# Kernel tuning notes

Measured on AMD Instinct MI355X. Metric: run time of the kernel, lower is better.

The kernel has to match this reference:

```python
import jax
import jax.numpy as jnp
from jax import lax
import numpy as np

EMBED_DIM = 768
NUM_HEADS = 12
BATCH = 8
SEQ = 1024
EPS = 1e-07
QK_QBIT = 8
QK_KBIT = 8
AV_ABIT = 8
AV_VBIT = 8
PROJ_WBIT = 8
PROJ_XBIT = 8
SCALE = EMBED_DIM ** (-0.5)  # module uses embed_dim, not head_dim


def _ste(hard, soft):
    # straight-through estimator: forward = hard, backward grad = d(soft)
    return soft + lax.stop_gradient(hard - soft)


def fake_quant_signed(x, bit):
    # _quantize_signed_matrix_train: sign/abs, global-max scaling, STE clamp + round
    sign = lax.stop_gradient(jnp.sign(x))
    a = jnp.abs(x)
    scaling = lax.stop_gradient(jnp.max(a)) + EPS
    y = a / scaling
    y = _ste(jnp.clip(y, 0.0, 1.0), y)          # Clamp.apply (STE)
    levels = 2.0 ** (bit - 1.0) - 1.0
    y = _ste(jnp.round(y * levels) / levels, y)  # Round.apply (STE)
    return y * scaling * sign


def fake_quant_unsigned(x, bit):
    # _quantize_unsigned_matrix_train
    scaling = lax.stop_gradient(jnp.max(x)) + EPS
    y = x / scaling
    y = _ste(jnp.clip(y, 0.0, 1.0), y)
    levels = 2.0 ** bit - 1.0
    y = _ste(jnp.round(y * levels) / levels, y)
    return y * scaling


def asim_linear(x, w, b, wbit, xbit):
    # ASiMLinear in 'Train' mode with signed_act=True: fake-quantize activation
    # and weight, dense matmul, trim_noise=0 -> no perturbation.
    xq = fake_quant_signed(x, xbit)
    wq = fake_quant_signed(w, wbit)
    return jnp.einsum('bnc,oc->bno', xq, wq) + b


def setup_inputs() -> dict:
    key = jax.random.key(0)
    k_x, k_qw, k_qb, k_pw, k_pb = jax.random.split(key, 5)
    x = jax.random.normal(k_x, (BATCH, SEQ, EMBED_DIM), dtype=jnp.float32)
    s = 1.0 / np.sqrt(EMBED_DIM)
    qkv_w = jax.random.normal(k_qw, (3 * EMBED_DIM, EMBED_DIM), dtype=jnp.float32) * s
    qkv_b = jax.random.normal(k_qb, (3 * EMBED_DIM,), dtype=jnp.float32) * 0.01
    proj_w = jax.random.normal(k_pw, (EMBED_DIM, EMBED_DIM), dtype=jnp.float32) * s
    proj_b = jax.random.normal(k_pb, (EMBED_DIM,), dtype=jnp.float32) * 0.01
    return {'x': x, 'qkv_w': qkv_w, 'qkv_b': qkv_b, 'proj_w': proj_w, 'proj_b': proj_b}


def reference(x, qkv_w, qkv_b, proj_w, proj_b):
    B, N, C = x.shape
    H = NUM_HEADS
    D = C // H
    # qkv projection (ASiMLinear, Train mode)
    qkv = asim_linear(x, qkv_w, qkv_b, PROJ_WBIT, PROJ_XBIT)      # [B, N, 3C]
    qkv = qkv.reshape(B, N, 3, H, D).transpose(2, 0, 3, 1, 4)      # [3, B, H, N, D]
    q, k, v = qkv[0], qkv[1], qkv[2]
    # _qk_train: fake-quantize q and k^T, matmul (trim_noise=0 -> no perturb)
    qq = fake_quant_signed(q, QK_QBIT)
    kq = fake_quant_signed(jnp.swapaxes(k, -2, -1), QK_KBIT)
    attn = jnp.einsum('bhnd,bhdm->bhnm', qq, kq) * SCALE           # [B, H, N, N]
    attn = jax.nn.softmax(attn, axis=-1)
    # dropout ratio 0.0 -> identity
    # _av_train: unsigned fake-quant of attention, signed fake-quant of v
    aq = fake_quant_unsigned(attn, AV_ABIT)
    vq = fake_quant_signed(v, AV_VBIT)
    out = jnp.einsum('bhnm,bhmd->bhnd', aq, vq)                    # [B, H, N, D]
    out = out.transpose(0, 2, 1, 3).reshape(B, N, C)
    # output projection (ASiMLinear, Train mode)
    out = asim_linear(out, proj_w, proj_b, PROJ_WBIT, PROJ_XBIT)
    return out
```

## Files before the change

kernel.cpp:

```cpp
#include <hip/hip_runtime.h>
#include <hip/hip_bf16.h>
#include <cstdint>
#include <cstddef>

#define B_    8
#define SEQ_  1024
#define C_    768
#define H_    12
#define D_    64
#define TC_   2304
#define M_    8192
#define EPS_  1e-7f
#define SCALE_ 0.036084391824351615f

typedef __attribute__((ext_vector_type(8))) short bf16x8;
typedef __attribute__((ext_vector_type(4))) float f32x4;
typedef __attribute__((ext_vector_type(4))) int   i32x4;

__device__ __forceinline__ bf16x8 expand8(int2 raw) {
  union { int2 v; signed char c[8]; } u; u.v = raw;
  bf16x8 r;
  #pragma unroll
  for (int j = 0; j < 8; ++j) {
    float f = (float)(int)u.c[j];
    r[j] = (short)(__float_as_uint(f) >> 16);
  }
  return r;
}
__device__ __forceinline__ void expand16(int4 raw, int4& lo, int4& hi) {
  union { int4 v; signed char c[16]; } u; u.v = raw;
  unsigned short s[16];
  #pragma unroll
  for (int j = 0; j < 16; ++j) {
    float f = (float)(int)u.c[j];
    s[j] = (unsigned short)(__float_as_uint(f) >> 16);
  }
  lo = *(const int4*)&s[0]; hi = *(const int4*)&s[8];
}

__device__ __forceinline__ int8_t quant1(float v, float s) {
  float y = fminf(fabsf(v) / s, 1.0f);
  int q = (int)rintf(y * 127.0f);
  return (int8_t)(v < 0.f ? -q : q);
}

__global__ void k_init(float* g) {
  if (threadIdx.x == 0) {
    g[0]=0.f; g[1]=0.f; g[2]=0.f; g[3]=0.f; g[4]=0.f; g[5]=0.f;
    g[6]=3.402823466e+38f;
    g[7]=0.f;
  }
}

__global__ __launch_bounds__(256) void k_absmax_fused(const float4* __restrict__ x,
                                                      const float4* __restrict__ w1,
                                                      const float4* __restrict__ w2,
                                                      float* g) {
  __shared__ float red[4];
  const int blk = blockIdx.x;
  const float4* p; unsigned n4; float* gout; int b0, nb;
  if (blk < 384)      { p = x;  n4 = 1572864u; gout = &g[0]; b0 = 0;   nb = 384; }
  else if (blk < 480) { p = w1; n4 = 442368u;  gout = &g[1]; b0 = 384; nb = 96;  }
  else                { p = w2; n4 = 147456u;  gout = &g[2]; b0 = 480; nb = 48;  }
  float m = 0.f;
  for (unsigned i = (unsigned)(blk - b0) * 256u + threadIdx.x; i < n4; i += (unsigned)nb * 256u) {
    float4 v = p[i];
    m = fmaxf(m, fmaxf(fmaxf(fabsf(v.x), fabsf(v.y)), fmaxf(fabsf(v.z), fabsf(v.w))));
  }
  #pragma unroll
  for (int off = 32; off; off >>= 1) m = fmaxf(m, __shfl_xor(m, off));
  if ((threadIdx.x & 63) == 0) red[threadIdx.x >> 6] = m;
  __syncthreads();
  if (threadIdx.x == 0) {
    m = fmaxf(fmaxf(red[0], red[1]), fmaxf(red[2], red[3]));
    atomicMax((unsigned int*)gout, __float_as_uint(m));
  }
}

__device__ __forceinline__ void quant_seg8(const float* __restrict__ in, unsigned n, float s,
                                           int8_t* __restrict__ out, unsigned i0, unsigned stride) {
  for (unsigned i = i0; i < n; i += stride)
    out[i] = quant1(in[i], s);
}
__global__ __launch_bounds__(256) void k_quant_fused(const float* __restrict__ x,
                                                     const float* __restrict__ w1,
                                                     const float* __restrict__ w2,
                                                     const float* __restrict__ g,
                                                     int8_t* __restrict__ xq,
                                                     int8_t* __restrict__ wq,
                                                     int8_t* __restrict__ pw) {
  const int blk = blockIdx.x;
  if (blk < 1536)      quant_seg8(x,  6291456u, g[0] + EPS_, xq, (unsigned)blk * 256u + threadIdx.x, 1536u * 256u);
  else if (blk < 1968) quant_seg8(w1, 1769472u, g[1] + EPS_, wq, (unsigned)(blk - 1536) * 256u + threadIdx.x, 432u * 256u);
  else                 quant_seg8(w2,  589824u, g[2] + EPS_, pw, (unsigned)(blk - 1968) * 256u + threadIdx.x, 144u * 256u);
}

__global__ __launch_bounds__(256) void k_quant_i8(const float* __restrict__ in, unsigned n,
                                                  const float* __restrict__ gmax,
                                                  int8_t* __restrict__ out) {
  const float s = *gmax + EPS_;
  quant_seg8(in, n, s, out, blockIdx.x * blockDim.x + threadIdx.x, gridDim.x * blockDim.x);
}

__global__ __launch_bounds__(256) void k_gemm8i(const int8_t* __restrict__ A,
                                                const int8_t* __restrict__ Bt,
                                                const float* __restrict__ bias,
                                                float* __restrict__ C,
                                                int Mn, int Nn, int Kn,
                                                const float* __restrict__ sA, const float* __restrict__ sB,
                                                float* pmax, int partDiv) {
  __shared__ int8_t As[4][128][16];
  __shared__ int8_t Bs[4][128][16];
  const int tid = threadIdx.x;
  int flat = blockIdx.y * gridDim.x + blockIdx.x;
  int chunk = (gridDim.x * gridDim.y) >> 3;
  int nf = (flat & 7) * chunk + (flat >> 3);
  const int n0 = (nf % gridDim.x) * 128, m0 = (nf / gridDim.x) * 128;
  const int wid = tid >> 6, lane = tid & 63;
  const int wr = wid >> 1, wc = wid & 1;
  const int lrow = lane & 15;
  const int lslot = lane >> 4;
  i32x4 acc[4][4] = {};
  const int srow = tid & 127;
  const int slot0 = tid >> 7;
  const int8_t* ga = A  + (size_t)(m0 + srow) * Kn + slot0 * 16;
  const int8_t* gb = Bt + (size_t)(n0 + srow) * Kn + slot0 * 16;
  const int nt = Kn >> 6;
  int4 ra0 = *(const int4*)(ga);
  int4 ra1 = *(const int4*)(ga + 32);
  int4 rb0 = *(const int4*)(gb);
  int4 rb1 = *(const int4*)(gb + 32);
  for (int t = 0; t < nt; ++t) {
    if (t) __syncthreads();
    *(int4*)&As[slot0][srow][0]     = ra0;
    *(int4*)&As[slot0 + 2][srow][0] = ra1;
    *(int4*)&Bs[slot0][srow][0]     = rb0;
    *(int4*)&Bs[slot0 + 2][srow][0] = rb1;
    if (t + 1 < nt) {
      const int ko = (t + 1) * 64;
      ra0 = *(const int4*)(ga + ko);
      ra1 = *(const int4*)(ga + ko + 32);
      rb0 = *(const int4*)(gb + ko);
      rb1 = *(const int4*)(gb + ko + 32);
    }
    __syncthreads();
    i32x4 af[4], bfr[4];
    #pragma unroll
    for (int i = 0; i < 4; ++i) af[i]  = *(const i32x4*)&As[lslot][wr * 64 + i * 16 + lrow][0];
    #pragma unroll
    for (int j = 0; j < 4; ++j) bfr[j] = *(const i32x4*)&Bs[lslot][wc * 64 + j * 16 + lrow][0];
    #pragma unroll
    for (int i = 0; i < 4; ++i)
      #pragma unroll
      for (int j = 0; j < 4; ++j)
        acc[i][j] = __builtin_amdgcn_mfma_i32_16x16x64_i8(af[i], bfr[j], acc[i][j], 0, 0, 0);
  }
  const float alpha = (sA[0] + EPS_) * (sB[0] + EPS_) * (1.0f / 16129.0f);
  const int orow = (lane >> 4) << 2;
  float amax = 0.f;
  #pragma unroll
  for (int i = 0; i < 4; ++i) {
    #pragma unroll
    for (int j = 0; j < 4; ++j) {
      int col = n0 + wc * 64 + j * 16 + lrow;
      float bc = bias[col];
      #pragma unroll
      for (int rr = 0; rr < 4; ++rr) {
        int row = m0 + wr * 64 + i * 16 + orow + rr;
        float val = (float)acc[i][j][rr] * alpha + bc;
        C[(size_t)row * Nn + col] = val;
        amax = fmaxf(amax, fabsf(val));
      }
    }
  }
  if (pmax) {
    #pragma unroll
    for (int off = 32; off; off >>= 1) amax = fmaxf(amax, __shfl_xor(amax, off));
    if (lane == 0) atomicMax((unsigned int*)&pmax[n0 / partDiv], __float_as_uint(amax));
  }
}

__global__ __launch_bounds__(256) void k_quant_heads(const float* __restrict__ qkvf, const float* __restrict__ g,
                                                     int8_t* __restrict__ qo, int8_t* __restrict__ ko,
                                                     int8_t* __restrict__ vT) {
  __shared__ float vt[64][65];
  const int bh = blockIdx.x >> 4, nt = blockIdx.x & 15;
  const int b = bh / 12, h = bh % 12;
  const int n0 = nt * 64;
  const int tid = threadIdx.x;
  const float s0 = g[3] + EPS_, s1 = g[4] + EPS_, s2 = g[5] + EPS_;
  const int r = tid >> 2, dc = tid & 3;
  const size_t mrow = (size_t)(b * 1024 + n0 + r) * 2304;
  union { int4 v; int8_t c[16]; } pk;
  {
    const float* src = qkvf + mrow + h * 64 + dc * 16;
    #pragma unroll
    for (int e = 0; e < 16; ++e) pk.c[e] = quant1(src[e], s0);
    *(int4*)&qo[((size_t)bh * 1024 + n0 + r) * 64 + dc * 16] = pk.v;
  }
  {
    const float* src = qkvf + mrow + 768 + h * 64 + dc * 16;
    #pragma unroll
    for (int e = 0; e < 16; ++e) pk.c[e] = quant1(src[e], s1);
    *(int4*)&ko[((size_t)bh * 1024 + n0 + r) * 64 + dc * 16] = pk.v;
  }
  {
    const float* src = qkvf + mrow + 1536 + h * 64 + dc * 16;
    #pragma unroll
    for (int e = 0; e < 16; ++e) vt[dc * 16 + e][r] = src[e];
  }
  __syncthreads();
  {
    const int d = tid >> 2, nc = tid & 3;
    #pragma unroll
    for (int e = 0; e < 16; ++e) pk.c[e] = quant1(vt[d][nc * 16 + e], s2);
    *(int4*)&vT[((size_t)bh * 64 + d) * 1024 + n0 + nc * 16] = pk.v;
  }
}

__global__ __launch_bounds__(256) void k_attn_stats_mfma(
    const int8_t* __restrict__ qi8, const int8_t* __restrict__ ki8,
    const float* __restrict__ g, float* __restrict__ rowmax, float* __restrict__ denomv,
    unsigned int* __restrict__ gminden) {
  __shared__ unsigned short Ks[64 * 64];
  __shared__ float red[4];
  const int bh = blockIdx.x >> 4, rt = blockIdx.x & 15;
  const int tid = threadIdx.x, w = tid >> 6, lane = tid & 63;
  const int lrow = lane & 15, lko = (lane >> 4) << 3;
  const int8_t* qbase = qi8 + (size_t)bh * 65536;
  const int8_t* kbase = ki8 + (size_t)bh * 65536;
  bf16x8 qf[2];
  #pragma unroll
  for (int ks = 0; ks < 2; ++ks)
    qf[ks] = expand8(*(const int2*)(qbase + (size_t)(rt*64 + w*16 + lrow) * 64 + ks*32 + lko));
  const float qkScale = (g[3] + EPS_) * (g[4] + EPS_) * (1.0f / 16129.0f) * SCALE_;
  float m = -3.0e38f, den = 0.f;
  const int srow = tid >> 2, sc = tid & 3;
  const int sx = (srow & 7) << 4;
  int4 kraw = *(const int4*)(kbase + (size_t)srow * 64 + sc * 16);
  for (int t = 0; t < 16; ++t) {
    __syncthreads();
    {
      int4 lo, hi; expand16(kraw, lo, hi);
      int bb = srow * 128 + sc * 32;
      *(int4*)((char*)Ks + ( bb       ^ sx)) = lo;
      *(int4*)((char*)Ks + ((bb + 16) ^ sx)) = hi;
    }
    if (t < 15)
      kraw = *(const int4*)(kbase + (size_t)(t + 1) * 4096 + (size_t)srow * 64 + sc * 16);
    __syncthreads();
    f32x4 acc[4] = {};
    #pragma unroll
    for (int ks = 0; ks < 2; ++ks)
      #pragma unroll
      for (int j = 0; j < 4; ++j) {
        int row = j * 16 + lrow;
        bf16x8 kf = *(const bf16x8*)((const char*)Ks + ((row * 128 + (ks*32 + lko) * 2) ^ ((row & 7) << 4)));
        acc[j] = __builtin_amdgcn_mfma_f32_16x16x32_bf16(kf, qf[ks], acc[j], 0, 0, 0);
      }
    float mnew = m;
    #pragma unroll
    for (int j = 0; j < 4; ++j)
      #pragma unroll
      for (int rr = 0; rr < 4; ++rr)
        mnew = fmaxf(mnew, acc[j][rr] * qkScale);
    float d = den * __expf(m - mnew);
    #pragma unroll
    for (int j = 0; j < 4; ++j)
      #pragma unroll
      for (int rr = 0; rr < 4; ++rr)
        d += __expf(acc[j][rr] * qkScale - mnew);
    den = d; m = mnew;
  }
  #pragma unroll
  for (int off = 16; off <= 32; off <<= 1) {
    float mo = __shfl_xor(m, off);
    float doo = __shfl_xor(den, off);
    float mg = fmaxf(m, mo);
    den = den * __expf(m - mg) + doo * __expf(mo - mg);
    m = mg;
  }
  if (lane < 16) {
    size_t rg = (size_t)bh * 1024 + rt * 64 + w * 16 + lane;
    rowmax[rg] = m;
    denomv[rg] = den;
  }
  float bm = den;
  #pragma unroll
  for (int off = 1; off < 16; off <<= 1) bm = fminf(bm, __shfl_xor(bm, off));
  if (lane == 0) red[w] = bm;
  __syncthreads();
  if (tid == 0)
    atomicMin(gminden, __float_as_uint(fminf(fminf(red[0], red[1]), fminf(red[2], red[3]))));
}

__global__ __launch_bounds__(256) void k_attn_pv_mfma(
    const int8_t* __restrict__ qi8, const int8_t* __restrict__ ki8, const int8_t* __restrict__ vti8,
    const float* __restrict__ g, const unsigned int* __restrict__ gminden,
    const float* __restrict__ rowmax, const float* __restrict__ denomv,
    float* __restrict__ aof, float* __restrict__ gamax) {
  __shared__ unsigned short Ks[64 * 64];
  __shared__ unsigned short Vs[64 * 64];
  __shared__ unsigned short Ps[64 * 64];
  __shared__ float red[4];
  const int bh = blockIdx.x >> 4, rt = blockIdx.x & 15;
  const int b = bh / 12, h = bh % 12;
  const int tid = threadIdx.x, w = tid >> 6, lane = tid & 63;
  const int lrow = lane & 15, lko = (lane >> 4) << 3;
  const int8_t* qbase = qi8 + (size_t)bh * 65536;
  const int8_t* kbase = ki8 + (size_t)bh * 65536;
  const int8_t* vbase = vti8 + (size_t)bh * 65536;
  bf16x8 qf[2];
  #pragma unroll
  for (int ks = 0; ks < 2; ++ks)
    qf[ks] = expand8(*(const int2*)(qbase + (size_t)(rt*64 + w*16 + lrow) * 64 + ks*32 + lko));
  const float qkScale = (g[3] + EPS_) * (g[4] + EPS_) * (1.0f / 16129.0f) * SCALE_;
  const float minden = __uint_as_float(*gminden);
  const float sa = 1.0f / minden + EPS_;
  const float invSa = 1.0f / sa;
  const float sv = g[5] + EPS_;
  const float pvScale = sa * sv * (1.0f / 32385.0f);
  const float rm  = rowmax[(size_t)bh * 1024 + rt * 64 + w * 16 + lrow];
  const float ivd = 1.0f / denomv[(size_t)bh * 1024 + rt * 64 + w * 16 + lrow];
  f32x4 accO[4] = {};
  const int srow = tid >> 2, sc = tid & 3;
  const int sx = (srow & 7) << 4;
  int4 kraw = *(const int4*)(kbase + (size_t)srow * 64 + sc * 16);
  int4 vraw = *(const int4*)(vbase + (size_t)srow * 1024 + sc * 16);
  for (int t = 0; t < 16; ++t) {
    __syncthreads();
    {
      int4 lo, hi;
      int bb = srow * 128 + sc * 32;
      expand16(kraw, lo, hi);
      *(int4*)((char*)Ks + ( bb       ^ sx)) = lo;
      *(int4*)((char*)Ks + ((bb + 16) ^ sx)) = hi;
      expand16(vraw, lo, hi);
      *(int4*)((char*)Vs + ( bb       ^ sx)) = lo;
      *(int4*)((char*)Vs + ((bb + 16) ^ sx)) = hi;
    }
    if (t < 15) {
      kraw = *(const int4*)(kbase + (size_t)(t + 1) * 4096 + (size_t)srow * 64 + sc * 16);
      vraw = *(const int4*)(vbase + (size_t)srow * 1024 + (t + 1) * 64 + sc * 16);
    }
    __syncthreads();
    f32x4 acc[4] = {};
    #pragma unroll
    for (int ks = 0; ks < 2; ++ks)
      #pragma unroll
      for (int j = 0; j < 4; ++j) {
        int row = j * 16 + lrow;
        bf16x8 kf = *(const bf16x8*)((const char*)Ks + ((row * 128 + (ks*32 + lko) * 2) ^ ((row & 7) << 4)));
        acc[j] = __builtin_amdgcn_mfma_f32_16x16x32_bf16(kf, qf[ks], acc[j], 0, 0, 0);
      }
    const int q = w * 16 + lrow;
    const int kb = (lane >> 4) << 2;
    #pragma unroll
    for (int j = 0; j < 4; ++j) {
      float a0 = rintf(fminf(__expf(acc[j][0] * qkScale - rm) * ivd * invSa, 1.0f) * 255.0f);
      float a1 = rintf(fminf(__expf(acc[j][1] * qkScale - rm) * ivd * invSa, 1.0f) * 255.0f);
      float a2 = rintf(fminf(__expf(acc[j][2] * qkScale - rm) * ivd * invSa, 1.0f) * 255.0f);
      float a3 = rintf(fminf(__expf(acc[j][3] * qkScale - rm) * ivd * invSa, 1.0f) * 255.0f);
      uint2 pk;
      pk.x = (__float_as_uint(a0) >> 16) | ((__float_as_uint(a1) >> 16) << 16);
      pk.y = (__float_as_uint(a2) >> 16) | ((__float_as_uint(a3) >> 16) << 16);
      int byteoff = (q * 128 + (j * 16 + kb) * 2) ^ ((q & 7) << 4);
      *(uint2*)((char*)Ps + byteoff) = pk;
    }
    #pragma unroll
    for (int ks = 0; ks < 2; ++ks) {
      bf16x8 pf = *(const bf16x8*)((const char*)Ps + ((q * 128 + (ks*32 + lko) * 2) ^ ((q & 7) << 4)));
      #pragma unroll
      for (int j = 0; j < 4; ++j) {
        int row = j * 16 + lrow;
        bf16x8 vf = *(const bf16x8*)((const char*)Vs + ((row * 128 + (ks*32 + lko) * 2) ^ ((row & 7) << 4)));
        accO[j] = __builtin_amdgcn_mfma_f32_16x16x32_bf16(pf, vf, accO[j], 0, 0, 0);
      }
    }
  }
  float amax = 0.f;
  #pragma unroll
  for (int j = 0; j < 4; ++j) {
    int d = j * 16 + lrow;
    #pragma unroll
    for (int rr = 0; rr < 4; ++rr) {
      int row = rt * 64 + w * 16 + (lane >> 4) * 4 + rr;
      float val = accO[j][rr] * pvScale;
      aof[((size_t)(b * 1024 + row)) * 768 + h * 64 + d] = val;
      amax = fmaxf(amax, fabsf(val));
    }
  }
  #pragma unroll
  for (int off = 1; off < 64; off <<= 1) amax = fmaxf(amax, __shfl_xor(amax, off));
  if (lane == 0) red[w] = amax;
  __syncthreads();
  if (tid == 0)
    atomicMax((unsigned int*)gamax, __float_as_uint(fmaxf(fmaxf(red[0], red[1]), fmaxf(red[2], red[3]))));
}

extern "C" void kernel_launch(void* const* d_in, const int* in_sizes, int n_in,
                              void* d_out, int out_size, void* d_ws, size_t ws_size,
                              hipStream_t stream) {
  const float* x      = (const float*)d_in[0];
  const float* qkv_w  = (const float*)d_in[1];
  const float* qkv_b  = (const float*)d_in[2];
  const float* proj_w = (const float*)d_in[3];
  const float* proj_b = (const float*)d_in[4];
  float* out = (float*)d_out;

  char* w = (char*)d_ws;
  float*          g      = (float*)(w + 0);
  float*          rowmax = (float*)(w + 256);
  float*          denomv = (float*)(w + 393472);
  int8_t*         qi8    = (int8_t*)(w + 786688);
  int8_t*         ki8    = (int8_t*)(w + 7078144);
  int8_t*         vT     = (int8_t*)(w + 13369600);
  int8_t*         pw8    = (int8_t*)(w + 19661056);
  int8_t*         xq8    = (int8_t*)(w + 20840704);
  int8_t*         wq8    = (int8_t*)(w + 33423616);
  float*          qkvf   = (float*)(w + 36962560);
  float*          aof    = (float*)(w + 36962560);
  int8_t*         aob8   = (int8_t*)(w + 62128384);

  hipLaunchKernelGGL(k_init, dim3(1), dim3(64), 0, stream, g);

  hipLaunchKernelGGL(k_absmax_fused, dim3(528), dim3(256), 0, stream,
                     (const float4*)x, (const float4*)qkv_w, (const float4*)proj_w, g);

  hipLaunchKernelGGL(k_quant_fused, dim3(2112), dim3(256), 0, stream,
                     x, qkv_w, proj_w, g, xq8, wq8, pw8);

  hipLaunchKernelGGL(k_gemm8i, dim3(TC_ / 128, M_ / 128), dim3(256), 0, stream,
                     xq8, wq8, qkv_b, qkvf, M_, TC_, C_, &g[0], &g[1], &g[3], 768);

  hipLaunchKernelGGL(k_quant_heads, dim3(1536), dim3(256), 0, stream, qkvf, g, qi8, ki8, vT);

  hipLaunchKernelGGL(k_attn_stats_mfma, dim3(1536), dim3(256), 0, stream,
                     qi8, ki8, g, rowmax, denomv, (unsigned int*)&g[6]);
  hipLaunchKernelGGL(k_attn_pv_mfma, dim3(1536), dim3(256), 0, stream,
                     qi8, ki8, vT, g, (const unsigned int*)&g[6], rowmax, denomv, aof, &g[7]);

  hipLaunchKernelGGL(k_quant_i8, dim3(2048), dim3(256), 0, stream, aof, 6291456u, &g[7], aob8);

  hipLaunchKernelGGL(k_gemm8i, dim3(C_ / 128, M_ / 128), dim3(256), 0, stream,
                     aob8, pw8, proj_b, out, M_, C_, C_, &g[7], &g[2], (float*)nullptr, 1);

  (void)in_sizes; (void)n_in; (void)out_size; (void)ws_size;
}
```

Measured before the change: 236.4 us.

## Load int8 GEMM MFMA fragments directly from global memory, bypassing LDS

The int8 GEMM no longer stages A and B tiles through shared memory with register double-buffering and barriers. Each lane reads its MFMA operand fragments directly from global memory inside an unrolled K loop. This removes LDS writes, LDS reads and both __syncthreads per K step. In exchange, tiles are fetched redundantly by the two waves sharing a row or column block, and global load latency is exposed without explicit prefetching.

```diff
diff --git a/kernel.cpp b/kernel.cpp
--- a/kernel.cpp
+++ b/kernel.cpp
@@ -109,8 +109,6 @@
                                                 int Mn, int Nn, int Kn,
                                                 const float* __restrict__ sA, const float* __restrict__ sB,
                                                 float* pmax, int partDiv) {
-  __shared__ int8_t As[4][128][16];
-  __shared__ int8_t Bs[4][128][16];
   const int tid = threadIdx.x;
   int flat = blockIdx.y * gridDim.x + blockIdx.x;
   int chunk = (gridDim.x * gridDim.y) >> 3;
@@ -121,34 +119,16 @@
   const int lrow = lane & 15;
   const int lslot = lane >> 4;
   i32x4 acc[4][4] = {};
-  const int srow = tid & 127;
-  const int slot0 = tid >> 7;
-  const int8_t* ga = A  + (size_t)(m0 + srow) * Kn + slot0 * 16;
-  const int8_t* gb = Bt + (size_t)(n0 + srow) * Kn + slot0 * 16;
-  const int nt = Kn >> 6;
-  int4 ra0 = *(const int4*)(ga);
-  int4 ra1 = *(const int4*)(ga + 32);
-  int4 rb0 = *(const int4*)(gb);
-  int4 rb1 = *(const int4*)(gb + 32);
-  for (int t = 0; t < nt; ++t) {
-    if (t) __syncthreads();
-    *(int4*)&As[slot0][srow][0]     = ra0;
-    *(int4*)&As[slot0 + 2][srow][0] = ra1;
-    *(int4*)&Bs[slot0][srow][0]     = rb0;
-    *(int4*)&Bs[slot0 + 2][srow][0] = rb1;
-    if (t + 1 < nt) {
-      const int ko = (t + 1) * 64;
-      ra0 = *(const int4*)(ga + ko);
-      ra1 = *(const int4*)(ga + ko + 32);
-      rb0 = *(const int4*)(gb + ko);
-      rb1 = *(const int4*)(gb + ko + 32);
-    }
-    __syncthreads();
+  const int8_t* pa = A  + (size_t)(m0 + wr * 64 + lrow) * Kn + lslot * 16;
+  const int8_t* pb = Bt + (size_t)(n0 + wc * 64 + lrow) * Kn + lslot * 16;
+  const size_t rs = (size_t)16 * Kn;
+  #pragma unroll 4
+  for (int k = 0; k < Kn; k += 64) {
     i32x4 af[4], bfr[4];
     #pragma unroll
-    for (int i = 0; i < 4; ++i) af[i]  = *(const i32x4*)&As[lslot][wr * 64 + i * 16 + lrow][0];
-    #pragma unroll
-    for (int j = 0; j < 4; ++j) bfr[j] = *(const i32x4*)&Bs[lslot][wc * 64 + j * 16 + lrow][0];
+    for (int i = 0; i < 4; ++i) af[i]  = *(const i32x4*)(pa + i * rs + k);
+    #pragma unroll
+    for (int j = 0; j < 4; ++j) bfr[j] = *(const i32x4*)(pb + j * rs + k);
     #pragma unroll
     for (int i = 0; i < 4; ++i)
       #pragma unroll
```

New measurement: 258.4 us. 1.09x slower.

## Recompute QKV GEMM to fuse per-part max and head quantization, skip fp32 store

Applied to the files above, without the earlier changes.

The QKV int8 GEMM now runs twice. The first pass only computes the per-part abs max with atomics. The second pass recomputes the GEMM and quantizes straight into the per-head q/k and transposed v int8 layouts. For q/k it swaps the MFMA operands so each lane writes contiguous d values. This removes the 75 MB fp32 qkv store and reload and the separate k_quant_heads kernel, at the cost of doing the GEMM compute twice. The output projection also moves to 64-row tiles, giving more blocks to fill the GPU.

```diff
diff --git a/kernel.cpp b/kernel.cpp
--- a/kernel.cpp
+++ b/kernel.cpp
@@ -102,120 +102,202 @@
   quant_seg8(in, n, s, out, blockIdx.x * blockDim.x + threadIdx.x, gridDim.x * blockDim.x);
 }
 
-__global__ __launch_bounds__(256) void k_gemm8i(const int8_t* __restrict__ A,
-                                                const int8_t* __restrict__ Bt,
-                                                const float* __restrict__ bias,
-                                                float* __restrict__ C,
-                                                int Mn, int Nn, int Kn,
-                                                const float* __restrict__ sA, const float* __restrict__ sB,
-                                                float* pmax, int partDiv) {
+#define GEMM_PROLOGUE()                                                        \
+  const int tid = threadIdx.x;                                                 \
+  int flat = blockIdx.y * gridDim.x + blockIdx.x;                              \
+  int chunk = (gridDim.x * gridDim.y) >> 3;                                    \
+  int nf = (flat & 7) * chunk + (flat >> 3);                                   \
+  const int n0 = (nf % gridDim.x) * 128, m0 = (nf / gridDim.x) * 128;          \
+  const int wid = tid >> 6, lane = tid & 63;                                   \
+  const int wr = wid >> 1, wc = wid & 1;                                       \
+  const int lrow = lane & 15;                                                  \
+  const int lslot = lane >> 4;                                                 \
+  const int srow = tid & 127;                                                  \
+  const int slot0 = tid >> 7;                                                  \
+  const int8_t* ga = A  + (size_t)(m0 + srow) * Kn + slot0 * 16;               \
+  const int8_t* gb = Bt + (size_t)(n0 + srow) * Kn + slot0 * 16;               \
+  const int nt = Kn >> 6;                                                      \
+  int4 ra0 = *(const int4*)(ga);                                               \
+  int4 ra1 = *(const int4*)(ga + 32);                                          \
+  int4 rb0 = *(const int4*)(gb);                                               \
+  int4 rb1 = *(const int4*)(gb + 32);
+
+#define GEMM_KLOOP(SWAP)                                                       \
+  for (int t = 0; t < nt; ++t) {                                               \
+    if (t) __syncthreads();                                                    \
+    *(int4*)&As[slot0][srow][0]     = ra0;                                     \
+    *(int4*)&As[slot0 + 2][srow][0] = ra1;                                     \
+    *(int4*)&Bs[slot0][srow][0]     = rb0;                                     \
+    *(int4*)&Bs[slot0 + 2][srow][0] = rb1;                                     \
+    if (t + 1 < nt) {                                                          \
+      const int ko = (t + 1) * 64;                                             \
+      ra0 = *(const int4*)(ga + ko);                                           \
+      ra1 = *(const int4*)(ga + ko + 32);                                      \
+      rb0 = *(const int4*)(gb + ko);                                           \
+      rb1 = *(const int4*)(gb + ko + 32);                                      \
+    }                                                                          \
+    __syncthreads();                                                           \
+    i32x4 af[4], bfr[4];                                                       \
+    _Pragma("unroll")                                                          \
+    for (int i = 0; i < 4; ++i) af[i]  = *(const i32x4*)&As[lslot][wr * 64 + i * 16 + lrow][0]; \
+    _Pragma("unroll")                                                          \
+    for (int j = 0; j < 4; ++j) bfr[j] = *(const i32x4*)&Bs[lslot][wc * 64 + j * 16 + lrow][0]; \
+    _Pragma("unroll")                                                          \
+    for (int i = 0; i < 4; ++i)                                                \
+      _Pragma("unroll")                                                        \
+      for (int j = 0; j < 4; ++j)                                              \
+        acc[i][j] = (SWAP) ? __builtin_amdgcn_mfma_i32_16x16x64_i8(bfr[j], af[i], acc[i][j], 0, 0, 0) \
+                           : __builtin_amdgcn_mfma_i32_16x16x64_i8(af[i], bfr[j], acc[i][j], 0, 0, 0); \
+  }
+
+__global__ __launch_bounds__(256) void k_gemm_max(const int8_t* __restrict__ A,
+                                                  const int8_t* __restrict__ Bt,
+                                                  const float* __restrict__ bias,
+                                                  int Kn,
+                                                  const float* __restrict__ sA, const float* __restrict__ sB,
+                                                  float* pmax) {
   __shared__ int8_t As[4][128][16];
+  __shared__ int8_t Bs[4][128][16];
+  i32x4 acc[4][4] = {};
+  GEMM_PROLOGUE()
+  GEMM_KLOOP(false)
+  const float alpha = (sA[0] + EPS_) * (sB[0] + EPS_) * (1.0f / 16129.0f);
+  float amax = 0.f;
+  #pragma unroll
+  for (int i = 0; i < 4; ++i)
+    #pragma unroll
+    for (int j = 0; j < 4; ++j) {
+      float bc = bias[n0 + wc * 64 + j * 16 + lrow];
+      #pragma unroll
+      for (int rr = 0; rr < 4; ++rr)
+        amax = fmaxf(amax, fabsf((float)acc[i][j][rr] * alpha + bc));
+    }
+  #pragma unroll
+  for (int off = 32; off; off >>= 1) amax = fmaxf(amax, __shfl_xor(amax, off));
+  if (lane == 0) atomicMax((unsigned int*)&pmax[n0 / 768], __float_as_uint(amax));
+  (void)m0; (void)lslot;
+}
+
+__global__ __launch_bounds__(256) void k_gemm_quant(const int8_t* __restrict__ A,
+                                                    const int8_t* __restrict__ Bt,
+                                                    const float* __restrict__ bias,
+                                                    int Kn, const float* __restrict__ g,
+                                                    int8_t* __restrict__ qo, int8_t* __restrict__ ko,
+                                                    int8_t* __restrict__ vT) {
+  __shared__ int8_t As[4][128][16];
+  __shared__ int8_t Bs[4][128][16];
+  i32x4 acc[4][4] = {};
+  GEMM_PROLOGUE()
+  const int part = n0 / 768;
+  if (part < 2) { GEMM_KLOOP(true) } else { GEMM_KLOOP(false) }
+  const float alpha = (g[0] + EPS_) * (g[1] + EPS_) * (1.0f / 16129.0f);
+  const float s = g[3 + part] + EPS_;
+  const int orow = (lane >> 4) << 2;
+  const int bb = m0 >> 10;
+  if (part < 2) {
+    int8_t* dst = part ? ko : qo;
+    #pragma unroll
+    for (int i = 0; i < 4; ++i) {
+      const int m = m0 + wr * 64 + i * 16 + lrow;
+      const int n = m & 1023;
+      #pragma unroll
+      for (int j = 0; j < 4; ++j) {
+        const int c0 = n0 + wc * 64 + j * 16 + orow;
+        const int hh = (c0 - part * 768) >> 6;
+        const int d0 = c0 & 63;
+        const float4 bv = *(const float4*)&bias[c0];
+        union { unsigned int u; int8_t c[4]; } pk;
+        pk.c[0] = quant1((float)acc[i][j][0] * alpha + bv.x, s);
+        pk.c[1] = quant1((float)acc[i][j][1] * alpha + bv.y, s);
+        pk.c[2] = quant1((float)acc[i][j][2] * alpha + bv.z, s);
+        pk.c[3] = quant1((float)acc[i][j][3] * alpha + bv.w, s);
+        *(unsigned int*)&dst[((size_t)(bb * 12 + hh) * 1024 + n) * 64 + d0] = pk.u;
+      }
+    }
+  } else {
+    #pragma unroll
+    for (int j = 0; j < 4; ++j) {
+      const int c = n0 + wc * 64 + j * 16 + lrow;
+      const int hh = (c - 1536) >> 6;
+      const int d = c & 63;
+      const float bc = bias[c];
+      #pragma unroll
+      for (int i = 0; i < 4; ++i) {
+        const int nb = (m0 & 1023) + wr * 64 + i * 16 + orow;
+        union { unsigned int u; int8_t c[4]; } pk;
+        pk.c[0] = quant1((float)acc[i][j][0] * alpha + bc, s);
+        pk.c[1] = quant1((float)acc[i][j][1] * alpha + bc, s);
+        pk.c[2] = quant1((float)acc[i][j][2] * alpha + bc, s);
+        pk.c[3] = quant1((float)acc[i][j][3] * alpha + bc, s);
+        *(unsigned int*)&vT[((size_t)(bb * 12 + hh) * 64 + d) * 1024 + nb] = pk.u;
+      }
+    }
+  }
+}
+
+__global__ __launch_bounds__(256) void k_gemm8i_64(const int8_t* __restrict__ A,
+                                                   const int8_t* __restrict__ Bt,
+                                                   const float* __restrict__ bias,
+                                                   float* __restrict__ C,
+                                                   int Nn, int Kn,
+                                                   const float* __restrict__ sA, const float* __restrict__ sB) {
+  __shared__ int8_t As[4][64][16];
   __shared__ int8_t Bs[4][128][16];
   const int tid = threadIdx.x;
   int flat = blockIdx.y * gridDim.x + blockIdx.x;
   int chunk = (gridDim.x * gridDim.y) >> 3;
   int nf = (flat & 7) * chunk + (flat >> 3);
-  const int n0 = (nf % gridDim.x) * 128, m0 = (nf / gridDim.x) * 128;
+  const int n0 = (nf % gridDim.x) * 128, m0 = (nf / gridDim.x) * 64;
   const int wid = tid >> 6, lane = tid & 63;
   const int wr = wid >> 1, wc = wid & 1;
   const int lrow = lane & 15;
   const int lslot = lane >> 4;
-  i32x4 acc[4][4] = {};
-  const int srow = tid & 127;
-  const int slot0 = tid >> 7;
-  const int8_t* ga = A  + (size_t)(m0 + srow) * Kn + slot0 * 16;
-  const int8_t* gb = Bt + (size_t)(n0 + srow) * Kn + slot0 * 16;
+  i32x4 acc[2][4] = {};
+  const int arow = tid & 63, aslot = tid >> 6;
+  const int brow = tid & 127, bslot0 = tid >> 7;
+  const int8_t* ga = A  + (size_t)(m0 + arow) * Kn + aslot * 16;
+  const int8_t* gb = Bt + (size_t)(n0 + brow) * Kn + bslot0 * 16;
   const int nt = Kn >> 6;
   int4 ra0 = *(const int4*)(ga);
-  int4 ra1 = *(const int4*)(ga + 32);
   int4 rb0 = *(const int4*)(gb);
   int4 rb1 = *(const int4*)(gb + 32);
   for (int t = 0; t < nt; ++t) {
     if (t) __syncthreads();
-    *(int4*)&As[slot0][srow][0]     = ra0;
-    *(int4*)&As[slot0 + 2][srow][0] = ra1;
-    *(int4*)&Bs[slot0][srow][0]     = rb0;
-    *(int4*)&Bs[slot0 + 2][srow][0] = rb1;
+    *(int4*)&As[aslot][arow][0]      = ra0;
+    *(int4*)&Bs[bslot0][brow][0]     = rb0;
+    *(int4*)&Bs[bslot0 + 2][brow][0] = rb1;
     if (t + 1 < nt) {
       const int ko = (t + 1) * 64;
       ra0 = *(const int4*)(ga + ko);
-      ra1 = *(const int4*)(ga + ko + 32);
       rb0 = *(const int4*)(gb + ko);
       rb1 = *(const int4*)(gb + ko + 32);
     }
     __syncthreads();
-    i32x4 af[4], bfr[4];
-    #pragma unroll
-    for (int i = 0; i < 4; ++i) af[i]  = *(const i32x4*)&As[lslot][wr * 64 + i * 16 + lrow][0];
+    i32x4 af[2], bfr[4];
+    #pragma unroll
+    for (int i = 0; i < 2; ++i) af[i]  = *(const i32x4*)&As[lslot][wr * 32 + i * 16 + lrow][0];
     #pragma unroll
     for (int j = 0; j < 4; ++j) bfr[j] = *(const i32x4*)&Bs[lslot][wc * 64 + j * 16 + lrow][0];
     #pragma unroll
-    for (int i = 0; i < 4; ++i)
+    for (int i = 0; i < 2; ++i)
       #pragma unroll
       for (int j = 0; j < 4; ++j)
         acc[i][j] = __builtin_amdgcn_mfma_i32_16x16x64_i8(af[i], bfr[j], acc[i][j], 0, 0, 0);
   }
   const float alpha = (sA[0] + EPS_) * (sB[0] + EPS_) * (1.0f / 16129.0f);
   const int orow = (lane >> 4) << 2;
-  float amax = 0.f;
-  #pragma unroll
-  for (int i = 0; i < 4; ++i) {
+  #pragma unroll
+  for (int i = 0; i < 2; ++i)
     #pragma unroll
     for (int j = 0; j < 4; ++j) {
-      int col = n0 + wc * 64 + j * 16 + lrow;
-      float bc = bias[col];
+      const int col = n0 + wc * 64 + j * 16 + lrow;
+      const float bc = bias[col];
       #pragma unroll
       for (int rr = 0; rr < 4; ++rr) {
-        int row = m0 + wr * 64 + i * 16 + orow + rr;
-        float val = (float)acc[i][j][rr] * alpha + bc;
-        C[(size_t)row * Nn + col] = val;
-        amax = fmaxf(amax, fabsf(val));
+        const int row = m0 + wr * 32 + i * 16 + orow + rr;
+        C[(size_t)row * Nn + col] = (float)acc[i][j][rr] * alpha + bc;
       }
     }
-  }
-  if (pmax) {
-    #pragma unroll
-    for (int off = 32; off; off >>= 1) amax = fmaxf(amax, __shfl_xor(amax, off));
-    if (lane == 0) atomicMax((unsigned int*)&pmax[n0 / partDiv], __float_as_uint(amax));
-  }
-}
-
-__global__ __launch_bounds__(256) void k_quant_heads(const float* __restrict__ qkvf, const float* __restrict__ g,
-                                                     int8_t* __restrict__ qo, int8_t* __restrict__ ko,
-                                                     int8_t* __restrict__ vT) {
-  __shared__ float vt[64][65];
-  const int bh = blockIdx.x >> 4, nt = blockIdx.x & 15;
-  const int b = bh / 12, h = bh % 12;
-  const int n0 = nt * 64;
-  const int tid = threadIdx.x;
-  const float s0 = g[3] + EPS_, s1 = g[4] + EPS_, s2 = g[5] + EPS_;
-  const int r = tid >> 2, dc = tid & 3;
-  const size_t mrow = (size_t)(b * 1024 + n0 + r) * 2304;
-  union { int4 v; int8_t c[16]; } pk;
-  {
-    const float* src = qkvf + mrow + h * 64 + dc * 16;
-    #pragma unroll
-    for (int e = 0; e < 16; ++e) pk.c[e] = quant1(src[e], s0);
-    *(int4*)&qo[((size_t)bh * 1024 + n0 + r) * 64 + dc * 16] = pk.v;
-  }
-  {
-    const float* src = qkvf + mrow + 768 + h * 64 + dc * 16;
-    #pragma unroll
-    for (int e = 0; e < 16; ++e) pk.c[e] = quant1(src[e], s1);
-    *(int4*)&ko[((size_t)bh * 1024 + n0 + r) * 64 + dc * 16] = pk.v;
-  }
-  {
-    const float* src = qkvf + mrow + 1536 + h * 64 + dc * 16;
-    #pragma unroll
-    for (int e = 0; e < 16; ++e) vt[dc * 16 + e][r] = src[e];
-  }
-  __syncthreads();
-  {
-    const int d = tid >> 2, nc = tid & 3;
-    #pragma unroll
-    for (int e = 0; e < 16; ++e) pk.c[e] = quant1(vt[d][nc * 16 + e], s2);
-    *(int4*)&vT[((size_t)bh * 64 + d) * 1024 + n0 + nc * 16] = pk.v;
-  }
 }
 
 __global__ __launch_bounds__(256) void k_attn_stats_mfma(
@@ -418,7 +500,6 @@
   int8_t*         pw8    = (int8_t*)(w + 19661056);
   int8_t*         xq8    = (int8_t*)(w + 20840704);
   int8_t*         wq8    = (int8_t*)(w + 33423616);
-  float*          qkvf   = (float*)(w + 36962560);
   float*          aof    = (float*)(w + 36962560);
   int8_t*         aob8   = (int8_t*)(w + 62128384);
 
@@ -430,10 +511,11 @@
   hipLaunchKernelGGL(k_quant_fused, dim3(2112), dim3(256), 0, stream,
                      x, qkv_w, proj_w, g, xq8, wq8, pw8);
 
-  hipLaunchKernelGGL(k_gemm8i, dim3(TC_ / 128, M_ / 128), dim3(256), 0, stream,
-                     xq8, wq8, qkv_b, qkvf, M_, TC_, C_, &g[0], &g[1], &g[3], 768);
-
-  hipLaunchKernelGGL(k_quant_heads, dim3(1536), dim3(256), 0, stream, qkvf, g, qi8, ki8, vT);
+  hipLaunchKernelGGL(k_gemm_max, dim3(TC_ / 128, M_ / 128), dim3(256), 0, stream,
+                     xq8, wq8, qkv_b, C_, &g[0], &g[1], &g[3]);
+
+  hipLaunchKernelGGL(k_gemm_quant, dim3(TC_ / 128, M_ / 128), dim3(256), 0, stream,
+                     xq8, wq8, qkv_b, C_, g, qi8, ki8, vT);
 
   hipLaunchKernelGGL(k_attn_stats_mfma, dim3(1536), dim3(256), 0, stream,
                      qi8, ki8, g, rowmax, denomv, (unsigned int*)&g[6]);
@@ -442,8 +524,8 @@
 
   hipLaunchKernelGGL(k_quant_i8, dim3(2048), dim3(256), 0, stream, aof, 6291456u, &g[7], aob8);
 
-  hipLaunchKernelGGL(k_gemm8i, dim3(C_ / 128, M_ / 128), dim3(256), 0, stream,
-                     aob8, pw8, proj_b, out, M_, C_, C_, &g[7], &g[2], (float*)nullptr, 1);
+  hipLaunchKernelGGL(k_gemm8i_64, dim3(C_ / 128, M_ / 64), dim3(256), 0, stream,
+                     aob8, pw8, proj_b, out, C_, C_, &g[7], &g[2]);
 
   (void)in_sizes; (void)n_in; (void)out_size; (void)ws_size;
 }
```

Result: slower. 256.5 us (+8.5%).
